# Performance work log

Measured on AMD Instinct MI355X. Metric: run time of the kernel, lower is better.

The kernel has to match this reference:

```python
import jax, jax.numpy as jnp
import numpy as np

OUT_SIZE = 224  # hardcoded in the torch forward: F.interpolate(size=224)


def _lin_interp_axis(x, axis, out_size):
    """1D linear interpolation along `axis` with align_corners=True."""
    in_size = x.shape[axis]
    # align_corners=True: src = dst * (in-1)/(out-1)
    pos = jnp.arange(out_size, dtype=jnp.float32) * ((in_size - 1) / (out_size - 1))
    i0 = jnp.clip(jnp.floor(pos).astype(jnp.int32), 0, in_size - 2)
    w = pos - i0.astype(jnp.float32)
    x0 = jnp.take(x, i0, axis=axis)
    x1 = jnp.take(x, i0 + 1, axis=axis)
    bshape = [1] * x.ndim
    bshape[axis] = out_size
    w = w.reshape(bshape)
    return x0 * (1.0 - w) + x1 * w


def setup_inputs() -> dict:
    key = jax.random.key(0)
    k1, k2, k3 = jax.random.split(key, 3)
    hidden, n_classes = 32, 4
    x = jax.random.normal(k1, (1, hidden, 14, 14, 14), dtype=jnp.float32)
    # 1x1x1 conv3d == per-voxel channel matmul; store kernel as [out, in]
    W = jax.random.normal(k2, (n_classes, hidden), dtype=jnp.float32) / np.sqrt(hidden)
    b = jax.random.normal(k3, (n_classes,), dtype=jnp.float32) * 0.01
    return {"x": x, "W": W, "b": b}


def reference(x, W, b):
    # Trilinear upsample (separable linear interp per spatial axis),
    # upsampling smallest dims first keeps peak memory low.
    y = _lin_interp_axis(x, 2, OUT_SIZE)   # [B,C,224,14,14]
    y = _lin_interp_axis(y, 3, OUT_SIZE)   # [B,C,224,224,14]
    y = _lin_interp_axis(y, 4, OUT_SIZE)   # [B,C,224,224,224]
    # 1x1x1 conv3d: per-voxel channel contraction
    z = jnp.einsum('bcdhw,oc->bodhw', y, W) + b[None, :, None, None, None]
    # softmax over channel dim (dim=1)
    return jax.nn.softmax(z, axis=1)
```

## Files before the change

### kernel.cpp

```cpp
#include <hip/hip_runtime.h>


#define NSP 2744
#define NPLANE 196
#define NV  11239424u
#define PLANE_OUT 50176u
#define RATIO (13.0f / 223.0f)
#define LOG2E 1.44269504088896340736f

__global__ __launch_bounds__(1024) void fused_decoder(
    const float* __restrict__ x,
    const float* __restrict__ W,
    const float* __restrict__ b,
    float* __restrict__ out)
{
    __shared__ float4 zloc[2 * NPLANE];
    __shared__ float4 etab[NPLANE];
    __shared__ float4 gtab[224 * 15];

    const int   t    = threadIdx.x;
    const unsigned dd = blockIdx.x;
    const float posd = (float)dd * RATIO;
    const int   i0d  = min((int)posd, 12);
    const float wd   = posd - (float)i0d;

    if (t < 2 * NPLANE) {
        int pl   = t / NPLANE;
        int s    = t - pl * NPLANE;
        int base = (i0d + pl) * NPLANE + s;
        float a0 = b[0], a1 = b[1], a2 = b[2], a3 = b[3];
#pragma unroll
        for (int c = 0; c < 32; ++c) {
            float xv = x[c * NSP + base];
            a0 = fmaf(W[c],      xv, a0);
            a1 = fmaf(W[32 + c], xv, a1);
            a2 = fmaf(W[64 + c], xv, a2);
            a3 = fmaf(W[96 + c], xv, a3);
        }
        zloc[t] = make_float4(a0, a1, a2, a3);
    }
    __syncthreads();

    if (t < NPLANE) {
        float4 z0 = zloc[t], z1 = zloc[NPLANE + t];
        float4 ev;
        ev.x = fmaf(wd, z1.x - z0.x, z0.x) * LOG2E;
        ev.y = fmaf(wd, z1.y - z0.y, z0.y) * LOG2E;
        ev.z = fmaf(wd, z1.z - z0.z, z0.z) * LOG2E;
        ev.w = fmaf(wd, z1.w - z0.w, z0.w) * LOG2E;
        etab[t] = ev;
    }
    __syncthreads();

    for (int k = t; k < 224 * 14; k += 1024) {
        int h  = k / 14;
        int iw = k - h * 14;
        float posh = (float)h * RATIO;
        int   i0h  = min((int)posh, 12);
        float wh   = posh - (float)i0h;
        float4 e0 = etab[i0h * 14 + iw];
        float4 e1 = etab[i0h * 14 + 14 + iw];
        float4 gv;
        gv.x = fmaf(wh, e1.x - e0.x, e0.x);
        gv.y = fmaf(wh, e1.y - e0.y, e0.y);
        gv.z = fmaf(wh, e1.z - e0.z, e0.z);
        gv.w = fmaf(wh, e1.w - e0.w, e0.w);
        gtab[h * 15 + iw] = gv;
    }
    __syncthreads();

    const unsigned planeBase = dd * PLANE_OUT;
    for (int g4 = t; g4 < 12544; g4 += 1024) {
        int w4 = g4 % 56;
        int h  = g4 / 56;
        int wb = w4 * 4;
        float posw0 = (float)wb * RATIO;
        int   iw0   = min((int)posw0, 12);
        float u     = posw0 - (float)iw0;
        int   gb    = h * 15 + iw0;
        int   iw2   = min(iw0 + 2, 13);
        float4 g0 = gtab[gb];
        float4 g1 = gtab[gb + 1];
        float4 g2 = gtab[h * 15 + iw2];

        float4 d10, d21;
        d10.x = g1.x - g0.x; d10.y = g1.y - g0.y; d10.z = g1.z - g0.z; d10.w = g1.w - g0.w;
        d21.x = g2.x - g1.x; d21.y = g2.y - g1.y; d21.z = g2.z - g1.z; d21.w = g2.w - g1.w;

        float4 res[4];
#pragma unroll
        for (int j = 0; j < 4; ++j) {
            float a  = fminf(u, 1.0f);
            float bb = u - a;
            float t0 = fmaf(bb, d21.x, fmaf(a, d10.x, g0.x));
            float t1 = fmaf(bb, d21.y, fmaf(a, d10.y, g0.y));
            float t2 = fmaf(bb, d21.z, fmaf(a, d10.z, g0.z));
            float t3 = fmaf(bb, d21.w, fmaf(a, d10.w, g0.w));
            float m  = fmaxf(fmaxf(t0, t1), fmaxf(t2, t3));
            float e0 = exp2f(t0 - m), e1 = exp2f(t1 - m);
            float e2 = exp2f(t2 - m), e3 = exp2f(t3 - m);
            float s  = (e0 + e1) + (e2 + e3);
            float inv = __builtin_amdgcn_rcpf(s);
            res[j].x = e0 * inv;
            res[j].y = e1 * inv;
            res[j].z = e2 * inv;
            res[j].w = e3 * inv;
            u += RATIO;
        }

        unsigned sidx = planeBase + (unsigned)h * 224u + (unsigned)wb;
        float4 o0 = make_float4(res[0].x, res[1].x, res[2].x, res[3].x);
        float4 o1 = make_float4(res[0].y, res[1].y, res[2].y, res[3].y);
        float4 o2 = make_float4(res[0].z, res[1].z, res[2].z, res[3].z);
        float4 o3 = make_float4(res[0].w, res[1].w, res[2].w, res[3].w);
        *(float4*)(out + 0u * NV + sidx) = o0;
        *(float4*)(out + 1u * NV + sidx) = o1;
        *(float4*)(out + 2u * NV + sidx) = o2;
        *(float4*)(out + 3u * NV + sidx) = o3;
    }
}

extern "C" void kernel_launch(void* const* d_in, const int* in_sizes, int n_in,
                              void* d_out, int out_size, void* d_ws, size_t ws_size,
                              hipStream_t stream) {
    const float* x = (const float*)d_in[0];
    const float* W = (const float*)d_in[1];
    const float* b = (const float*)d_in[2];
    float* out = (float*)d_out;
    (void)d_ws; (void)ws_size;

    fused_decoder<<<224, 1024, 0, stream>>>(x, W, b, out);
}
```

Measured before the change: 183.4 us.

## Split each depth plane into 8-row bands across many small blocks with staged stores

The grid changes from 224 blocks of 1024 threads (one per output depth plane) to 6272 blocks of 256 threads, each covering an 8-row band of a plane. The depth interpolation now happens on the input before the channel contraction, and only the few source rows a band needs are computed. Results go into a shared-memory staging buffer and are then written out as contiguous float4 runs per channel. This targets the low block count on a large GPU and aims for more coalesced stores, but it redoes the per-band channel contraction with redundant global reads and adds a synchronisation.

```diff
diff --git a/kernel.cpp b/kernel.cpp
--- a/kernel.cpp
+++ b/kernel.cpp
@@ -8,80 +8,78 @@
 #define RATIO (13.0f / 223.0f)
 #define LOG2E 1.44269504088896340736f
 
-__global__ __launch_bounds__(1024) void fused_decoder(
+__global__ __launch_bounds__(256) void fused_decoder(
     const float* __restrict__ x,
     const float* __restrict__ W,
     const float* __restrict__ b,
     float* __restrict__ out)
 {
-    __shared__ float4 zloc[2 * NPLANE];
-    __shared__ float4 etab[NPLANE];
-    __shared__ float4 gtab[224 * 15];
+    __shared__ float4 etab[4][14];
+    __shared__ float4 gtab[8][15];
+    __shared__ float4 stg[4][8][56];
 
-    const int   t    = threadIdx.x;
-    const unsigned dd = blockIdx.x;
+    const int t    = threadIdx.x;
+    const int bid  = blockIdx.x;
+    const int dd   = bid / 28;
+    const int band = bid - dd * 28;
+    const int h0   = band * 8;
+
     const float posd = (float)dd * RATIO;
     const int   i0d  = min((int)posd, 12);
     const float wd   = posd - (float)i0d;
 
-    if (t < 2 * NPLANE) {
-        int pl   = t / NPLANE;
-        int s    = t - pl * NPLANE;
-        int base = (i0d + pl) * NPLANE + s;
+    const float posh0 = (float)h0 * RATIO;
+    const int   hs0   = min((int)posh0, 12);
+
+    if (t < 56) {
+        int j  = t / 14;
+        int iw = t - j * 14;
+        int sr = min(hs0 + j, 13);
+        int base0 = (i0d * 14 + sr) * 14 + iw;
+        int base1 = base0 + NPLANE;
         float a0 = b[0], a1 = b[1], a2 = b[2], a3 = b[3];
 #pragma unroll
         for (int c = 0; c < 32; ++c) {
-            float xv = x[c * NSP + base];
+            float x0 = x[c * NSP + base0];
+            float x1 = x[c * NSP + base1];
+            float xv = fmaf(wd, x1 - x0, x0);
             a0 = fmaf(W[c],      xv, a0);
             a1 = fmaf(W[32 + c], xv, a1);
             a2 = fmaf(W[64 + c], xv, a2);
             a3 = fmaf(W[96 + c], xv, a3);
         }
-        zloc[t] = make_float4(a0, a1, a2, a3);
+        etab[j][iw] = make_float4(a0 * LOG2E, a1 * LOG2E, a2 * LOG2E, a3 * LOG2E);
     }
     __syncthreads();
 
-    if (t < NPLANE) {
-        float4 z0 = zloc[t], z1 = zloc[NPLANE + t];
-        float4 ev;
-        ev.x = fmaf(wd, z1.x - z0.x, z0.x) * LOG2E;
-        ev.y = fmaf(wd, z1.y - z0.y, z0.y) * LOG2E;
-        ev.z = fmaf(wd, z1.z - z0.z, z0.z) * LOG2E;
-        ev.w = fmaf(wd, z1.w - z0.w, z0.w) * LOG2E;
-        etab[t] = ev;
-    }
-    __syncthreads();
-
-    for (int k = t; k < 224 * 14; k += 1024) {
-        int h  = k / 14;
-        int iw = k - h * 14;
+    if (t < 112) {
+        int hl = t / 14;
+        int iw = t - hl * 14;
+        int h  = h0 + hl;
         float posh = (float)h * RATIO;
         int   i0h  = min((int)posh, 12);
         float wh   = posh - (float)i0h;
-        float4 e0 = etab[i0h * 14 + iw];
-        float4 e1 = etab[i0h * 14 + 14 + iw];
+        int   j    = i0h - hs0;
+        float4 e0 = etab[j][iw], e1 = etab[j + 1][iw];
         float4 gv;
         gv.x = fmaf(wh, e1.x - e0.x, e0.x);
         gv.y = fmaf(wh, e1.y - e0.y, e0.y);
         gv.z = fmaf(wh, e1.z - e0.z, e0.z);
         gv.w = fmaf(wh, e1.w - e0.w, e0.w);
-        gtab[h * 15 + iw] = gv;
+        gtab[hl][iw] = gv;
     }
     __syncthreads();
 
-    const unsigned planeBase = dd * PLANE_OUT;
-    for (int g4 = t; g4 < 12544; g4 += 1024) {
-        int w4 = g4 % 56;
-        int h  = g4 / 56;
+    for (int it = t; it < 448; it += 256) {
+        int hl = it / 56;
+        int w4 = it - hl * 56;
         int wb = w4 * 4;
         float posw0 = (float)wb * RATIO;
         int   iw0   = min((int)posw0, 12);
         float u     = posw0 - (float)iw0;
-        int   gb    = h * 15 + iw0;
-        int   iw2   = min(iw0 + 2, 13);
-        float4 g0 = gtab[gb];
-        float4 g1 = gtab[gb + 1];
-        float4 g2 = gtab[h * 15 + iw2];
+        float4 g0 = gtab[hl][iw0];
+        float4 g1 = gtab[hl][iw0 + 1];
+        float4 g2 = gtab[hl][min(iw0 + 2, 13)];
 
         float4 d10, d21;
         d10.x = g1.x - g0.x; d10.y = g1.y - g0.y; d10.z = g1.z - g0.z; d10.w = g1.w - g0.w;
@@ -108,15 +106,21 @@
             u += RATIO;
         }
 
-        unsigned sidx = planeBase + (unsigned)h * 224u + (unsigned)wb;
-        float4 o0 = make_float4(res[0].x, res[1].x, res[2].x, res[3].x);
-        float4 o1 = make_float4(res[0].y, res[1].y, res[2].y, res[3].y);
-        float4 o2 = make_float4(res[0].z, res[1].z, res[2].z, res[3].z);
-        float4 o3 = make_float4(res[0].w, res[1].w, res[2].w, res[3].w);
-        *(float4*)(out + 0u * NV + sidx) = o0;
-        *(float4*)(out + 1u * NV + sidx) = o1;
-        *(float4*)(out + 2u * NV + sidx) = o2;
-        *(float4*)(out + 3u * NV + sidx) = o3;
+        stg[0][hl][w4] = make_float4(res[0].x, res[1].x, res[2].x, res[3].x);
+        stg[1][hl][w4] = make_float4(res[0].y, res[1].y, res[2].y, res[3].y);
+        stg[2][hl][w4] = make_float4(res[0].z, res[1].z, res[2].z, res[3].z);
+        stg[3][hl][w4] = make_float4(res[0].w, res[1].w, res[2].w, res[3].w);
+    }
+    __syncthreads();
+
+    const float4* s = &stg[0][0][0];
+    const unsigned base = (unsigned)dd * PLANE_OUT + (unsigned)h0 * 224u;
+#pragma unroll
+    for (int k = 0; k < 7; ++k) {
+        int idx = k * 256 + t;
+        int c   = idx / 448;
+        int r   = idx - c * 448;
+        *(float4*)(out + (unsigned)c * NV + base + (unsigned)r * 4u) = s[idx];
     }
 }
 
@@ -129,5 +133,5 @@
     float* out = (float*)d_out;
     (void)d_ws; (void)ws_size;
 
-    fused_decoder<<<224, 1024, 0, stream>>>(x, W, b, out);
+    fused_decoder<<<224 * 28, 256, 0, stream>>>(x, W, b, out);
 }
```

Result: slower. 196.2 us (+7.0%).
